# Optimization experiments

Hardware: AMD Instinct MI355X
Metric: run time of the kernel (lower is better)

## Reference

```python
import jax, jax.numpy as jnp
import numpy as np

N, MAX_DEG, F_IN, F_OUT = 20000, 32, 128, 128
TRIM_RATIO = 0.45
N_NEIGH_THRESHOLD = 3


def setup_inputs() -> dict:
    key = jax.random.key(0)
    k_h, k_nbr, k_deg, k_w, k_b = jax.random.split(key, 5)
    h = jax.random.normal(k_h, (N, F_IN), dtype=jnp.float32)
    nbr = jax.random.randint(k_nbr, (N, MAX_DEG), 0, N, dtype=jnp.int32)
    # in-degree in [1, MAX_DEG] so every node has at least one neighbor
    deg = jax.random.randint(k_deg, (N,), 1, MAX_DEG + 1, dtype=jnp.int32)
    # GCN symmetric normalizer deg^-0.5, per node, shape [N, 1]
    norm = (deg.astype(jnp.float32) ** -0.5)[:, None]
    stdv = 1.0 / np.sqrt(F_OUT)
    weight = jax.random.uniform(k_w, (F_IN, F_OUT), jnp.float32, -stdv, stdv)
    bias = jax.random.uniform(k_b, (F_OUT,), jnp.float32, -stdv, stdv)
    return {"h": h, "norm": norm, "weight": weight, "bias": bias,
            "nbr": nbr, "deg": deg}


def reference(h, norm, weight, bias, nbr, deg):
    # h: [N,F] node features (dropout=0 so input_ft == dropped_h == h)
    # nbr: [N,D] padded src indices; deg: [N] valid neighbor counts; norm: [N,1]
    D = nbr.shape[1]
    slot = jnp.arange(D, dtype=deg.dtype)[None, :]            # [1,D]
    valid = slot < deg[:, None]                                # [N,D]

    h_nbr = h[nbr]                                             # [N,D,F] = mailbox input_ft
    msg = h_nbr * norm[nbr]                                    # [N,D,F] = mailbox m (src h * src norm)

    # padded slots -> +inf so they sort past all valid entries (ranks >= deg)
    big = jnp.asarray(jnp.finfo(h.dtype).max, h.dtype)
    ift = jnp.where(valid[..., None], h_nbr, big)
    sidx = jnp.argsort(ift, axis=1)                            # per-feature sort over neighbors
    gathered = jnp.take_along_axis(msg, sidx, axis=1)          # [N,D,F]

    n = deg                                                    # per-node n_neigh
    b_raw = n // 2 - (1 - n % 2)
    b_cap = jnp.floor(n.astype(jnp.float32) * TRIM_RATIO).astype(n.dtype)
    b = jnp.maximum(jnp.minimum(b_raw, b_cap), 1)              # trim count per node

    # keep sorted ranks in [b, n-b)
    sel = (slot >= b[:, None]) & (slot < (n - b)[:, None])     # [N,D]
    trimmed_sum = jnp.sum(gathered * sel[..., None].astype(h.dtype), axis=1)  # [N,F]

    self0 = h * norm                                           # dst h * dst norm (mailbox 'self'[:,0])
    alpha = (2 * b).astype(h.dtype)[:, None]
    accum_med = (trimmed_sum + self0 * alpha) * norm           # trim_compensate=True branch
    accum_small = (n.astype(h.dtype)[:, None] * self0) * norm  # n_neigh <= threshold branch
    accum = jnp.where((n <= N_NEIGH_THRESHOLD)[:, None], accum_small, accum_med)

    # NodeApplyModule_V2: linear + bias + relu
    out = jax.nn.relu(accum @ weight + bias)
    return out
```

## Files before the change

### kernel.cpp

```cpp
#include <hip/hip_runtime.h>
#include <cfloat>
#include <cmath>

#define N_NODES 20000
#define MAXD 32
#define F 128


template <int SZ>
__device__ __forceinline__ void oe_sort(float (&a)[SZ]) {
#pragma unroll
  for (int p = 1; p < SZ; p <<= 1) {
#pragma unroll
    for (int q = p; q >= 1; q >>= 1) {
#pragma unroll
      for (int j = q % p; j <= SZ - 1 - q; j += 2 * q) {
#pragma unroll
        for (int i = 0; i < q; ++i) {
          int x = i + j, y = i + j + q;
          if (y < SZ && (x / (2 * p)) == (y / (2 * p))) {
            float mn = fminf(a[x], a[y]);
            float mx = fmaxf(a[x], a[y]);
            a[x] = mn;
            a[y] = mx;
          }
        }
      }
    }
  }
}

template <int SZ>
__device__ __forceinline__ float extract_pos(const float (&k)[SZ], int p) {
  float sel[SZ];
#pragma unroll
  for (int i = 0; i < SZ; ++i) sel[i] = k[i];
#pragma unroll
  for (int w = SZ >> 1; w >= 1; w >>= 1) {
    bool take = (p & w) != 0;
#pragma unroll
    for (int i = 0; i < w; ++i) sel[i] = take ? sel[i + w] : sel[i];
  }
  return sel[0];
}

template <int SZ>
__device__ __forceinline__ float trimmed_sum(const float* __restrict__ h,
                                             const float* __restrict__ norm,
                                             const int* __restrict__ nbr_row,
                                             int n, int f, int b) {
  float ko[SZ];
  float nrm[SZ];
#pragma unroll
  for (int d = 0; d < SZ; ++d) {
    if (d < n) {
      int src = nbr_row[d];
      nrm[d] = norm[src];
      ko[d] = h[src * F + f];
    } else {
      nrm[d] = 0.f;
      ko[d] = FLT_MAX;
    }
  }

  float k[SZ];
#pragma unroll
  for (int d = 0; d < SZ; ++d) k[d] = ko[d];
  oe_sort<SZ>(k);

  const float lo  = extract_pos<SZ>(k, b);
  const float hi  = extract_pos<SZ>(k, n - b - 1);
  const float lom = extract_pos<SZ>(k, b - 1);
  const float him = extract_pos<SZ>(k, n - b);

  float sum = 0.f;
  if ((lom < lo) & (hi < him)) {
#pragma unroll
    for (int d = 0; d < SZ; ++d) {
      bool keep = (ko[d] >= lo) & (ko[d] <= hi);
      sum = fmaf(keep ? ko[d] : 0.f, nrm[d], sum);
    }
  } else {
    int c_lt_lo = 0, c_lt_hi = 0;
#pragma unroll
    for (int d = 0; d < SZ; ++d) {
      c_lt_lo += (ko[d] < lo) ? 1 : 0;
      c_lt_hi += (ko[d] < hi) ? 1 : 0;
    }
    int run_lo = 0, run_hi = 0;
    const int nb = n - b;
#pragma unroll
    for (int d = 0; d < SZ; ++d) {
      const float kd = ko[d];
      const float m = kd * nrm[d];
      const bool eql = (kd == lo);
      const bool eqh = (kd == hi);
      const bool lh = (lo < hi);
      const bool btw = (kd > lo) & (kd < hi);
      const int r_lo = c_lt_lo + run_lo;
      const int r_hi = c_lt_hi + run_hi;
      const bool inc = btw
                     | (eql & (r_lo >= b) & (lh | (r_lo < nb)))
                     | (lh & eqh & (r_hi < nb));
      sum += inc ? m : 0.f;
      run_lo += eql ? 1 : 0;
      run_hi += eqh ? 1 : 0;
    }
  }
  return sum;
}

__global__ __launch_bounds__(128) void gcn_stage1(const float* __restrict__ h,
                                                  const float* __restrict__ norm,
                                                  const int* __restrict__ nbr,
                                                  const int* __restrict__ deg,
                                                  float* __restrict__ accum) {
  const int i = blockIdx.x;
  const int f = threadIdx.x;
  const int n = deg[i];
  const float ni = norm[i];
  const float hif = h[i * F + f];
  const int idx = i * F + f;

  if (n <= 3) {
    accum[idx] = (float)n * hif * ni * ni;
    return;
  }

  int b = n / 2 - (1 - (n & 1));
  int bcap = (int)floorf((float)n * 0.45f);
  b = b < bcap ? b : bcap;
  b = b > 1 ? b : 1;

  const int* nbr_row = nbr + i * MAXD;
  float ts;
  if (n <= 4)       ts = trimmed_sum<4>(h, norm, nbr_row, n, f, b);
  else if (n <= 8)  ts = trimmed_sum<8>(h, norm, nbr_row, n, f, b);
  else if (n <= 16) ts = trimmed_sum<16>(h, norm, nbr_row, n, f, b);
  else              ts = trimmed_sum<32>(h, norm, nbr_row, n, f, b);

  accum[idx] = (ts + hif * ni * (float)(2 * b)) * ni;
}

__global__ __launch_bounds__(256) void gcn_gemm(const float* __restrict__ A,
                                                const float* __restrict__ W,
                                                const float* __restrict__ bias,
                                                float* __restrict__ out) {
  __shared__ float Ws[32 * F];
  __shared__ float As[32 * 36];
  const int t = threadIdx.x;
  const int tx = t & 31;
  const int ty = t >> 5;
  const int row0 = blockIdx.x * 32;
  const int ar = t >> 3, ak = t & 7;

  float acc[4][4];
#pragma unroll
  for (int r = 0; r < 4; ++r)
#pragma unroll
    for (int c = 0; c < 4; ++c) acc[r][c] = 0.f;

#pragma unroll
  for (int kc = 0; kc < F; kc += 32) {
    __syncthreads();
    float4 av = *(const float4*)(A + (row0 + ar) * F + kc + ak * 4);
    *(float4*)(As + ar * 36 + ak * 4) = av;
#pragma unroll
    for (int u = 0; u < 4; ++u) {
      int idx2 = u * 256 + t;
      *(float4*)(Ws + idx2 * 4) = *(const float4*)(W + kc * F + idx2 * 4);
    }
    __syncthreads();
#pragma unroll 8
    for (int k = 0; k < 32; ++k) {
      float4 w4 = *(const float4*)(Ws + k * F + tx * 4);
      float a0 = As[(ty * 4 + 0) * 36 + k];
      float a1 = As[(ty * 4 + 1) * 36 + k];
      float a2 = As[(ty * 4 + 2) * 36 + k];
      float a3 = As[(ty * 4 + 3) * 36 + k];
      acc[0][0] = fmaf(a0, w4.x, acc[0][0]); acc[0][1] = fmaf(a0, w4.y, acc[0][1]);
      acc[0][2] = fmaf(a0, w4.z, acc[0][2]); acc[0][3] = fmaf(a0, w4.w, acc[0][3]);
      acc[1][0] = fmaf(a1, w4.x, acc[1][0]); acc[1][1] = fmaf(a1, w4.y, acc[1][1]);
      acc[1][2] = fmaf(a1, w4.z, acc[1][2]); acc[1][3] = fmaf(a1, w4.w, acc[1][3]);
      acc[2][0] = fmaf(a2, w4.x, acc[2][0]); acc[2][1] = fmaf(a2, w4.y, acc[2][1]);
      acc[2][2] = fmaf(a2, w4.z, acc[2][2]); acc[2][3] = fmaf(a2, w4.w, acc[2][3]);
      acc[3][0] = fmaf(a3, w4.x, acc[3][0]); acc[3][1] = fmaf(a3, w4.y, acc[3][1]);
      acc[3][2] = fmaf(a3, w4.z, acc[3][2]); acc[3][3] = fmaf(a3, w4.w, acc[3][3]);
    }
  }

  float4 bv = *(const float4*)(bias + tx * 4);
#pragma unroll
  for (int r = 0; r < 4; ++r) {
    float4 o;
    o.x = fmaxf(acc[r][0] + bv.x, 0.f);
    o.y = fmaxf(acc[r][1] + bv.y, 0.f);
    o.z = fmaxf(acc[r][2] + bv.z, 0.f);
    o.w = fmaxf(acc[r][3] + bv.w, 0.f);
    *(float4*)(out + (row0 + ty * 4 + r) * F + tx * 4) = o;
  }
}

extern "C" void kernel_launch(void* const* d_in, const int* in_sizes, int n_in,
                              void* d_out, int out_size, void* d_ws, size_t ws_size,
                              hipStream_t stream) {
  const float* h = (const float*)d_in[0];
  const float* norm = (const float*)d_in[1];
  const float* weight = (const float*)d_in[2];
  const float* bias = (const float*)d_in[3];
  const int* nbr = (const int*)d_in[4];
  const int* deg = (const int*)d_in[5];
  float* out = (float*)d_out;
  float* accum = (float*)d_ws;

  gcn_stage1<<<N_NODES, 128, 0, stream>>>(h, norm, nbr, deg, accum);
  gcn_gemm<<<N_NODES / 32, 256, 0, stream>>>(accum, weight, bias, out);
}
```

Before: 134.9 us.

## Finer degree buckets, linear select extraction, vectorized GEMM A loads

```diff
diff --git a/kernel.cpp b/kernel.cpp
--- a/kernel.cpp
+++ b/kernel.cpp
@@ -32,16 +32,10 @@
 
 template <int SZ>
 __device__ __forceinline__ float extract_pos(const float (&k)[SZ], int p) {
-  float sel[SZ];
-#pragma unroll
-  for (int i = 0; i < SZ; ++i) sel[i] = k[i];
-#pragma unroll
-  for (int w = SZ >> 1; w >= 1; w >>= 1) {
-    bool take = (p & w) != 0;
-#pragma unroll
-    for (int i = 0; i < w; ++i) sel[i] = take ? sel[i + w] : sel[i];
-  }
-  return sel[0];
+  float sel = k[0];
+#pragma unroll
+  for (int i = 1; i < SZ; ++i) sel = (p == i) ? k[i] : sel;
+  return sel;
 }
 
 template <int SZ>
@@ -136,7 +130,11 @@
   float ts;
   if (n <= 4)       ts = trimmed_sum<4>(h, norm, nbr_row, n, f, b);
   else if (n <= 8)  ts = trimmed_sum<8>(h, norm, nbr_row, n, f, b);
+  else if (n <= 12) ts = trimmed_sum<12>(h, norm, nbr_row, n, f, b);
   else if (n <= 16) ts = trimmed_sum<16>(h, norm, nbr_row, n, f, b);
+  else if (n <= 20) ts = trimmed_sum<20>(h, norm, nbr_row, n, f, b);
+  else if (n <= 24) ts = trimmed_sum<24>(h, norm, nbr_row, n, f, b);
+  else if (n <= 28) ts = trimmed_sum<28>(h, norm, nbr_row, n, f, b);
   else              ts = trimmed_sum<32>(h, norm, nbr_row, n, f, b);
 
   accum[idx] = (ts + hif * ni * (float)(2 * b)) * ni;
@@ -160,7 +158,7 @@
 #pragma unroll
     for (int c = 0; c < 4; ++c) acc[r][c] = 0.f;
 
-#pragma unroll
+#pragma unroll 1
   for (int kc = 0; kc < F; kc += 32) {
     __syncthreads();
     float4 av = *(const float4*)(A + (row0 + ar) * F + kc + ak * 4);
@@ -171,21 +169,32 @@
       *(float4*)(Ws + idx2 * 4) = *(const float4*)(W + kc * F + idx2 * 4);
     }
     __syncthreads();
-#pragma unroll 8
-    for (int k = 0; k < 32; ++k) {
-      float4 w4 = *(const float4*)(Ws + k * F + tx * 4);
-      float a0 = As[(ty * 4 + 0) * 36 + k];
-      float a1 = As[(ty * 4 + 1) * 36 + k];
-      float a2 = As[(ty * 4 + 2) * 36 + k];
-      float a3 = As[(ty * 4 + 3) * 36 + k];
-      acc[0][0] = fmaf(a0, w4.x, acc[0][0]); acc[0][1] = fmaf(a0, w4.y, acc[0][1]);
-      acc[0][2] = fmaf(a0, w4.z, acc[0][2]); acc[0][3] = fmaf(a0, w4.w, acc[0][3]);
-      acc[1][0] = fmaf(a1, w4.x, acc[1][0]); acc[1][1] = fmaf(a1, w4.y, acc[1][1]);
-      acc[1][2] = fmaf(a1, w4.z, acc[1][2]); acc[1][3] = fmaf(a1, w4.w, acc[1][3]);
-      acc[2][0] = fmaf(a2, w4.x, acc[2][0]); acc[2][1] = fmaf(a2, w4.y, acc[2][1]);
-      acc[2][2] = fmaf(a2, w4.z, acc[2][2]); acc[2][3] = fmaf(a2, w4.w, acc[2][3]);
-      acc[3][0] = fmaf(a3, w4.x, acc[3][0]); acc[3][1] = fmaf(a3, w4.y, acc[3][1]);
-      acc[3][2] = fmaf(a3, w4.z, acc[3][2]); acc[3][3] = fmaf(a3, w4.w, acc[3][3]);
+#pragma unroll
+    for (int kq = 0; kq < 8; ++kq) {
+      float4 w0 = *(const float4*)(Ws + (kq * 4 + 0) * F + tx * 4);
+      float4 w1 = *(const float4*)(Ws + (kq * 4 + 1) * F + tx * 4);
+      float4 w2 = *(const float4*)(Ws + (kq * 4 + 2) * F + tx * 4);
+      float4 w3 = *(const float4*)(Ws + (kq * 4 + 3) * F + tx * 4);
+#pragma unroll
+      for (int r = 0; r < 4; ++r) {
+        float4 a = *(const float4*)(As + (ty * 4 + r) * 36 + kq * 4);
+        acc[r][0] = fmaf(a.x, w0.x, acc[r][0]);
+        acc[r][1] = fmaf(a.x, w0.y, acc[r][1]);
+        acc[r][2] = fmaf(a.x, w0.z, acc[r][2]);
+        acc[r][3] = fmaf(a.x, w0.w, acc[r][3]);
+        acc[r][0] = fmaf(a.y, w1.x, acc[r][0]);
+        acc[r][1] = fmaf(a.y, w1.y, acc[r][1]);
+        acc[r][2] = fmaf(a.y, w1.z, acc[r][2]);
+        acc[r][3] = fmaf(a.y, w1.w, acc[r][3]);
+        acc[r][0] = fmaf(a.z, w2.x, acc[r][0]);
+        acc[r][1] = fmaf(a.z, w2.y, acc[r][1]);
+        acc[r][2] = fmaf(a.z, w2.z, acc[r][2]);
+        acc[r][3] = fmaf(a.z, w2.w, acc[r][3]);
+        acc[r][0] = fmaf(a.w, w3.x, acc[r][0]);
+        acc[r][1] = fmaf(a.w, w3.y, acc[r][1]);
+        acc[r][2] = fmaf(a.w, w3.z, acc[r][2]);
+        acc[r][3] = fmaf(a.w, w3.w, acc[r][3]);
+      }
     }
   }
 
```

Measured after the change: 217.9 us. 1.62x slower.
